# Kernel optimization log

Measured on AMD Instinct MI355X. Metric: run time of the kernel, lower is better.

## Reference

```python
import jax, jax.numpy as jnp
import numpy as np

B, IN_DIM, LATENT_DIM, EMBED_DIM = 262144, 512, 128, 10000


def setup_inputs() -> dict:
    key = jax.random.key(0)
    k_x, k_y, k_wlv, k_blv, k_wmu, k_bmu, k_we, k_be = jax.random.split(key, 8)
    s_in = 1.0 / np.sqrt(IN_DIM)
    s_e = 1.0 / np.sqrt(EMBED_DIM)
    return {
        "x": jax.random.normal(k_x, (B, IN_DIM), dtype=jnp.float32),
        "y": jax.random.randint(k_y, (B,), 0, EMBED_DIM, dtype=jnp.int32),
        # torch nn.Linear weights are [out_features, in_features]
        "W_logvar": jax.random.uniform(k_wlv, (LATENT_DIM, IN_DIM), minval=-s_in, maxval=s_in, dtype=jnp.float32),
        "b_logvar": jax.random.uniform(k_blv, (LATENT_DIM,), minval=-s_in, maxval=s_in, dtype=jnp.float32),
        "W_mean": jax.random.uniform(k_wmu, (LATENT_DIM, IN_DIM), minval=-s_in, maxval=s_in, dtype=jnp.float32),
        "b_mean": jax.random.uniform(k_bmu, (LATENT_DIM,), minval=-s_in, maxval=s_in, dtype=jnp.float32),
        "W_embed": jax.random.uniform(k_we, (LATENT_DIM, EMBED_DIM), minval=-s_e, maxval=s_e, dtype=jnp.float32),
        "b_embed": jax.random.uniform(k_be, (LATENT_DIM,), minval=-s_e, maxval=s_e, dtype=jnp.float32),
    }


def reference(x, y, W_logvar, b_logvar, W_mean, b_mean, W_embed, b_embed):
    # logvar / mean heads: plain dense GEMMs, x @ W.T + b
    logvar = jnp.einsum("bi,li->bl", x, W_logvar) + b_logvar
    mean = jnp.einsum("bi,li->bl", x, W_mean) + b_mean
    # one_hot(y) @ W_embed.T + b_embed  ==  gather columns of W_embed at y
    embed = jnp.take(W_embed, y, axis=1).T + b_embed  # [B, latent_dim]
    return (logvar, mean, embed)
```

## Files before the change

kernel.cpp:

```cpp
#include <hip/hip_runtime.h>
#include <hip/hip_bf16.h>

#define NB 262144
#define KD 512
#define ED 10000

typedef __attribute__((ext_vector_type(8))) short s8v;
typedef __attribute__((ext_vector_type(4))) float f4v;

typedef __attribute__((address_space(1))) const unsigned int gu32_t;
typedef __attribute__((address_space(3))) unsigned int lu32_t;

__device__ __forceinline__ short f2bf(float f) {
  union { __hip_bfloat16 h; short s; } u;
  u.h = __float2bfloat16(f);
  return u.s;
}

__global__ void prep_all(const float* __restrict__ Wlv, const float* __restrict__ Wmu,
                         unsigned short* __restrict__ wbf,
                         const float* __restrict__ We, const float* __restrict__ be,
                         float* __restrict__ embT) {
  __shared__ float t[32][129];
  if (blockIdx.x < 512) {
    int i = blockIdx.x * 256 + threadIdx.x;
    int row = i >> 9, col = i & 511;
    float v = (row < 128) ? Wlv[(row << 9) | col] : Wmu[((row - 128) << 9) | col];
    union { __hip_bfloat16 h; unsigned short s; } u;
    u.h = __float2bfloat16(v);
    wbf[i] = u.s;
  } else {
    const int v0 = (blockIdx.x - 512) << 5;
#pragma unroll
    for (int j = 0; j < 16; ++j) {
      int idx = j * 256 + threadIdx.x;
      int l = idx >> 5, vi = idx & 31;
      int v = v0 + vi;
      t[vi][l] = (v < ED) ? We[(size_t)l * ED + v] : 0.f;
    }
    __syncthreads();
#pragma unroll
    for (int j = 0; j < 16; ++j) {
      int idx = j * 256 + threadIdx.x;
      int v = idx >> 7, l = idx & 127;
      if (v0 + v < ED)
        embT[(size_t)(v0 + v) * 128 + l] = t[v][l] + be[l];
    }
  }
}

__global__ __launch_bounds__(512, 4) void gemm_heads(
    const float* __restrict__ x, const unsigned short* __restrict__ wbf,
    const float* __restrict__ blv, const float* __restrict__ bmu,
    const int* __restrict__ y, const float* __restrict__ embT,
    float* __restrict__ out, int doEmbed) {
  __shared__ char lds[3 * 24576];
  const int tid  = threadIdx.x;
  const int lane = tid & 63;
  const int wid  = tid >> 6;
  const int wm   = wid >> 2;
  const int wn   = wid & 3;
  const int gm   = blockIdx.x << 6;
  const int lr   = lane & 15;
  const int kg   = lane >> 4;

  const int arow = tid >> 3, aq = tid & 7;
  const unsigned aSrcBase = (unsigned)(arow << 9) + (unsigned)((aq ^ (arow & 7)) << 2);
  const unsigned aDst = (unsigned)(tid << 4);
  unsigned bSrcBase[2], bDst[2];
#pragma unroll
  for (int s = 0; s < 2; ++s) {
    int c = tid + (s << 9);
    int col = c >> 2, q = c & 3;
    int qp = q ^ ((col >> 1) & 3);
    bSrcBase[s] = (unsigned)(col << 9) + (unsigned)(qp << 3);
    bDst[s] = 8192u + (unsigned)(c << 4);
  }
  const float* xblk = x + ((size_t)gm << 9);

  unsigned offA[2][2], offB[4];
#pragma unroll
  for (int m = 0; m < 2; ++m) {
    int row = (wm << 5) + (m << 4) + lr;
    int sw = row & 7;
    offA[m][0] = (unsigned)(row << 7) + (unsigned)((((kg << 1))     ^ sw) << 4);
    offA[m][1] = (unsigned)(row << 7) + (unsigned)((((kg << 1) + 1) ^ sw) << 4);
  }
#pragma unroll
  for (int nt = 0; nt < 4; ++nt) {
    int col = (wn << 6) + (nt << 4) + lr;
    offB[nt] = 8192u + (unsigned)(col << 6) + (unsigned)((kg ^ ((col >> 1) & 3)) << 4);
  }

  f4v acc[2][4];
#pragma unroll
  for (int m = 0; m < 2; ++m)
#pragma unroll
    for (int nt = 0; nt < 4; ++nt) acc[m][nt] = (f4v)0.f;

#define ISSUE_STAGE(st)                                                            \
  {                                                                                \
    const int ke = (st) << 5;                                                      \
    char* sb = lds + ((st) % 3) * 24576;                                           \
    __builtin_amdgcn_global_load_lds((const gu32_t*)(xblk + aSrcBase + ke),        \
                                     (lu32_t*)(sb + aDst), 16, 0, 0);              \
    __builtin_amdgcn_global_load_lds((const gu32_t*)(wbf + bSrcBase[0] + ke),      \
                                     (lu32_t*)(sb + bDst[0]), 16, 0, 0);           \
    __builtin_amdgcn_global_load_lds((const gu32_t*)(wbf + bSrcBase[1] + ke),      \
                                     (lu32_t*)(sb + bDst[1]), 16, 0, 0);           \
  }

  ISSUE_STAGE(0)
  ISSUE_STAGE(1)
  asm volatile("s_waitcnt vmcnt(3)" ::: "memory");
  __builtin_amdgcn_s_barrier();

#pragma unroll
  for (int t = 0; t < 16; ++t) {
    if (t <= 13) ISSUE_STAGE(t + 2)
    const char* stage = lds + (t % 3) * 24576;
    s8v bfr[4];
#pragma unroll
    for (int nt = 0; nt < 4; ++nt)
      bfr[nt] = *(const s8v*)(stage + offB[nt]);
    s8v af[2];
#pragma unroll
    for (int m = 0; m < 2; ++m) {
      float4 a0 = *(const float4*)(stage + offA[m][0]);
      float4 a1 = *(const float4*)(stage + offA[m][1]);
      af[m][0] = f2bf(a0.x); af[m][1] = f2bf(a0.y); af[m][2] = f2bf(a0.z); af[m][3] = f2bf(a0.w);
      af[m][4] = f2bf(a1.x); af[m][5] = f2bf(a1.y); af[m][6] = f2bf(a1.z); af[m][7] = f2bf(a1.w);
    }
#pragma unroll
    for (int m = 0; m < 2; ++m)
#pragma unroll
      for (int nt = 0; nt < 4; ++nt)
        acc[m][nt] = __builtin_amdgcn_mfma_f32_16x16x32_bf16(af[m], bfr[nt], acc[m][nt], 0, 0, 0);
    asm volatile("s_waitcnt lgkmcnt(0)" ::: "memory");
    __builtin_amdgcn_sched_barrier(0);
    if (t <= 13)      { asm volatile("s_waitcnt vmcnt(3)" ::: "memory"); }
    else if (t == 14) { asm volatile("s_waitcnt vmcnt(0)" ::: "memory"); }
    if (t <= 14) __builtin_amdgcn_s_barrier();
  }
#undef ISSUE_STAGE

  const int rsub = kg << 2;
#pragma unroll
  for (int nt = 0; nt < 4; ++nt) {
    int col = (wn << 6) + (nt << 4) + lr;
    float bias = (col < 128) ? blv[col] : bmu[col - 128];
    float* ob = (col < 128) ? (out + col)
                            : (out + ((size_t)NB << 7) + (col - 128));
#pragma unroll
    for (int m = 0; m < 2; ++m) {
      int row0 = gm + (wm << 5) + (m << 4) + rsub;
#pragma unroll
      for (int r = 0; r < 4; ++r)
        ob[(size_t)(row0 + r) << 7] = acc[m][nt][r] + bias;
    }
  }

  if (doEmbed) {
    float* out3 = out + ((size_t)NB << 8);
    int r  = tid >> 3;
    int c0 = (tid & 7) << 4;
    int row = gm + r;
    int v = y[row];
    const float4* src = (const float4*)(embT + (size_t)v * 128 + c0);
    float4* dst = (float4*)(out + ((size_t)NB << 8) - ((size_t)NB << 8) + ((size_t)row << 7) + c0 + ((size_t)NB << 8) - ((size_t)row << 7) - c0 + ((size_t)row << 7) + c0);
    dst = (float4*)(out3 + ((size_t)row << 7) + c0);
#pragma unroll
    for (int j = 0; j < 4; ++j) dst[j] = src[j];
  }
}

__global__ void gemm_naive(const float* __restrict__ x,
                           const float* __restrict__ Wlv, const float* __restrict__ blv,
                           const float* __restrict__ Wmu, const float* __restrict__ bmu,
                           float* __restrict__ out) {
  __shared__ float xr[512];
  int b = blockIdx.x;
  for (int i = threadIdx.x; i < 512; i += 256) xr[i] = x[(size_t)b * 512 + i];
  __syncthreads();
  int c = threadIdx.x;
  const float* w = (c < 128) ? (Wlv + c * 512) : (Wmu + (c - 128) * 512);
  float s = 0.f;
  for (int k = 0; k < 512; ++k) s += xr[k] * w[k];
  s += (c < 128) ? blv[c] : bmu[c - 128];
  float* o = (c < 128) ? (out + (size_t)b * 128 + c)
                       : (out + ((size_t)NB << 7) + (size_t)b * 128 + (c - 128));
  *o = s;
}

__global__ void embed_direct(const int* __restrict__ y, const float* __restrict__ We,
                             const float* __restrict__ be, float* __restrict__ out3) {
  size_t t = (size_t)blockIdx.x * 256 + threadIdx.x;
  int b = (int)(t >> 7), l = (int)(t & 127);
  out3[t] = We[(size_t)l * ED + y[b]] + be[l];
}

extern "C" void kernel_launch(void* const* d_in, const int* in_sizes, int n_in,
                              void* d_out, int out_size, void* d_ws, size_t ws_size,
                              hipStream_t stream) {
  const float* x   = (const float*)d_in[0];
  const int*   y   = (const int*)d_in[1];
  const float* Wlv = (const float*)d_in[2];
  const float* blv = (const float*)d_in[3];
  const float* Wmu = (const float*)d_in[4];
  const float* bmu = (const float*)d_in[5];
  const float* We  = (const float*)d_in[6];
  const float* be  = (const float*)d_in[7];
  float* out  = (float*)d_out;
  float* out3 = out + ((size_t)NB << 8);

  const size_t needW = 256 * 512 * sizeof(unsigned short);
  const size_t needE = needW + (size_t)ED * 128 * sizeof(float);
  unsigned short* wbf = (unsigned short*)d_ws;
  float* embT = (float*)((char*)d_ws + needW);

  if (ws_size >= needE) {
    prep_all<<<512 + 313, 256, 0, stream>>>(Wlv, Wmu, wbf, We, be, embT);
    gemm_heads<<<NB / 64, 512, 0, stream>>>(x, wbf, blv, bmu, y, embT, out, 1);
  } else if (ws_size >= needW) {
    prep_all<<<512, 256, 0, stream>>>(Wlv, Wmu, wbf, We, be, (float*)d_ws);
    gemm_heads<<<NB / 64, 512, 0, stream>>>(x, wbf, blv, bmu, y, nullptr, out, 0);
    embed_direct<<<NB * 128 / 256, 256, 0, stream>>>(y, We, be, out3);
  } else {
    gemm_naive<<<NB, 256, 0, stream>>>(x, Wlv, blv, Wmu, bmu, out);
    embed_direct<<<NB * 128 / 256, 256, 0, stream>>>(y, We, be, out3);
  }
}
```

Measured before the change: 296.9 us.

## Split GEMM output columns across two workgroups with XCD-aware block remapping

Each 64-row block is now handled by two workgroups, one per head (logvar vs mean), halving the B tile, accumulators and LDS footprint so launch bounds can allow more resident workgroups. Block IDs are remapped so the two halves of a row block land on the same XCD and can share the x tile through L2. The cost is that x is loaded twice per row block, which raises L2 and possibly HBM traffic on an input-bandwidth-bound kernel. The embedding copy is done only by the first half.

Measured after the change: 298.5 us. No clear change (+0.5%).

```diff
diff --git a/kernel.cpp b/kernel.cpp
--- a/kernel.cpp
+++ b/kernel.cpp
@@ -49,36 +49,35 @@
   }
 }
 
-__global__ __launch_bounds__(512, 4) void gemm_heads(
+__global__ __launch_bounds__(512, 6) void gemm_heads(
     const float* __restrict__ x, const unsigned short* __restrict__ wbf,
     const float* __restrict__ blv, const float* __restrict__ bmu,
     const int* __restrict__ y, const float* __restrict__ embT,
     float* __restrict__ out, int doEmbed) {
-  __shared__ char lds[3 * 24576];
+  __shared__ char lds[3 * 16384];
   const int tid  = threadIdx.x;
   const int lane = tid & 63;
   const int wid  = tid >> 6;
   const int wm   = wid >> 2;
   const int wn   = wid & 3;
-  const int gm   = blockIdx.x << 6;
+  const unsigned orig = blockIdx.x;
+  const unsigned wg   = (orig & 7u) * 1024u + (orig >> 3);
+  const int rb = (int)(wg >> 1);
+  const int h  = (int)(wg & 1);
+  const int gm   = rb << 6;
+  const int gcol = h << 7;
   const int lr   = lane & 15;
   const int kg   = lane >> 4;
 
   const int arow = tid >> 3, aq = tid & 7;
-  const unsigned aSrcBase = (unsigned)(arow << 9) + (unsigned)((aq ^ (arow & 7)) << 2);
+  const unsigned aSrc = (unsigned)(arow << 9) + (unsigned)((aq ^ (arow & 7)) << 2);
   const unsigned aDst = (unsigned)(tid << 4);
-  unsigned bSrcBase[2], bDst[2];
-#pragma unroll
-  for (int s = 0; s < 2; ++s) {
-    int c = tid + (s << 9);
-    int col = c >> 2, q = c & 3;
-    int qp = q ^ ((col >> 1) & 3);
-    bSrcBase[s] = (unsigned)(col << 9) + (unsigned)(qp << 3);
-    bDst[s] = 8192u + (unsigned)(c << 4);
-  }
+  const int bcol = tid >> 2, bq = tid & 3;
+  const unsigned bSrc = (unsigned)((gcol + bcol) << 9) + (unsigned)((bq ^ ((bcol >> 1) & 3)) << 3);
+  const unsigned bDst = 8192u + (unsigned)(tid << 4);
   const float* xblk = x + ((size_t)gm << 9);
 
-  unsigned offA[2][2], offB[4];
+  unsigned offA[2][2], offB[2];
 #pragma unroll
   for (int m = 0; m < 2; ++m) {
     int row = (wm << 5) + (m << 4) + lr;
@@ -87,41 +86,39 @@
     offA[m][1] = (unsigned)(row << 7) + (unsigned)((((kg << 1) + 1) ^ sw) << 4);
   }
 #pragma unroll
-  for (int nt = 0; nt < 4; ++nt) {
-    int col = (wn << 6) + (nt << 4) + lr;
+  for (int nt = 0; nt < 2; ++nt) {
+    int col = (wn << 5) + (nt << 4) + lr;
     offB[nt] = 8192u + (unsigned)(col << 6) + (unsigned)((kg ^ ((col >> 1) & 3)) << 4);
   }
 
-  f4v acc[2][4];
+  f4v acc[2][2];
 #pragma unroll
   for (int m = 0; m < 2; ++m)
 #pragma unroll
-    for (int nt = 0; nt < 4; ++nt) acc[m][nt] = (f4v)0.f;
+    for (int nt = 0; nt < 2; ++nt) acc[m][nt] = (f4v)0.f;
 
 #define ISSUE_STAGE(st)                                                            \
   {                                                                                \
     const int ke = (st) << 5;                                                      \
-    char* sb = lds + ((st) % 3) * 24576;                                           \
-    __builtin_amdgcn_global_load_lds((const gu32_t*)(xblk + aSrcBase + ke),        \
+    char* sb = lds + ((st) % 3) * 16384;                                           \
+    __builtin_amdgcn_global_load_lds((const gu32_t*)(xblk + aSrc + ke),            \
                                      (lu32_t*)(sb + aDst), 16, 0, 0);              \
-    __builtin_amdgcn_global_load_lds((const gu32_t*)(wbf + bSrcBase[0] + ke),      \
-                                     (lu32_t*)(sb + bDst[0]), 16, 0, 0);           \
-    __builtin_amdgcn_global_load_lds((const gu32_t*)(wbf + bSrcBase[1] + ke),      \
-                                     (lu32_t*)(sb + bDst[1]), 16, 0, 0);           \
+    __builtin_amdgcn_global_load_lds((const gu32_t*)(wbf + bSrc + ke),             \
+                                     (lu32_t*)(sb + bDst), 16, 0, 0);              \
   }
 
   ISSUE_STAGE(0)
   ISSUE_STAGE(1)
-  asm volatile("s_waitcnt vmcnt(3)" ::: "memory");
+  asm volatile("s_waitcnt vmcnt(2)" ::: "memory");
   __builtin_amdgcn_s_barrier();
 
 #pragma unroll
   for (int t = 0; t < 16; ++t) {
     if (t <= 13) ISSUE_STAGE(t + 2)
-    const char* stage = lds + (t % 3) * 24576;
-    s8v bfr[4];
-#pragma unroll
-    for (int nt = 0; nt < 4; ++nt)
+    const char* stage = lds + (t % 3) * 16384;
+    s8v bfr[2];
+#pragma unroll
+    for (int nt = 0; nt < 2; ++nt)
       bfr[nt] = *(const s8v*)(stage + offB[nt]);
     s8v af[2];
 #pragma unroll
@@ -134,11 +131,11 @@
 #pragma unroll
     for (int m = 0; m < 2; ++m)
 #pragma unroll
-      for (int nt = 0; nt < 4; ++nt)
+      for (int nt = 0; nt < 2; ++nt)
         acc[m][nt] = __builtin_amdgcn_mfma_f32_16x16x32_bf16(af[m], bfr[nt], acc[m][nt], 0, 0, 0);
     asm volatile("s_waitcnt lgkmcnt(0)" ::: "memory");
     __builtin_amdgcn_sched_barrier(0);
-    if (t <= 13)      { asm volatile("s_waitcnt vmcnt(3)" ::: "memory"); }
+    if (t <= 13)      { asm volatile("s_waitcnt vmcnt(2)" ::: "memory"); }
     else if (t == 14) { asm volatile("s_waitcnt vmcnt(0)" ::: "memory"); }
     if (t <= 14) __builtin_amdgcn_s_barrier();
   }
@@ -146,8 +143,8 @@
 
   const int rsub = kg << 2;
 #pragma unroll
-  for (int nt = 0; nt < 4; ++nt) {
-    int col = (wn << 6) + (nt << 4) + lr;
+  for (int nt = 0; nt < 2; ++nt) {
+    int col = gcol + (wn << 5) + (nt << 4) + lr;
     float bias = (col < 128) ? blv[col] : bmu[col - 128];
     float* ob = (col < 128) ? (out + col)
                             : (out + ((size_t)NB << 7) + (col - 128));
@@ -160,15 +157,14 @@
     }
   }
 
-  if (doEmbed) {
+  if (doEmbed && h == 0) {
     float* out3 = out + ((size_t)NB << 8);
     int r  = tid >> 3;
     int c0 = (tid & 7) << 4;
     int row = gm + r;
     int v = y[row];
     const float4* src = (const float4*)(embT + (size_t)v * 128 + c0);
-    float4* dst = (float4*)(out + ((size_t)NB << 8) - ((size_t)NB << 8) + ((size_t)row << 7) + c0 + ((size_t)NB << 8) - ((size_t)row << 7) - c0 + ((size_t)row << 7) + c0);
-    dst = (float4*)(out3 + ((size_t)row << 7) + c0);
+    float4* dst = (float4*)(out3 + ((size_t)row << 7) + c0);
 #pragma unroll
     for (int j = 0; j < 4; ++j) dst[j] = src[j];
   }
@@ -220,10 +216,10 @@
 
   if (ws_size >= needE) {
     prep_all<<<512 + 313, 256, 0, stream>>>(Wlv, Wmu, wbf, We, be, embT);
-    gemm_heads<<<NB / 64, 512, 0, stream>>>(x, wbf, blv, bmu, y, embT, out, 1);
+    gemm_heads<<<NB / 32, 512, 0, stream>>>(x, wbf, blv, bmu, y, embT, out, 1);
   } else if (ws_size >= needW) {
     prep_all<<<512, 256, 0, stream>>>(Wlv, Wmu, wbf, We, be, (float*)d_ws);
-    gemm_heads<<<NB / 64, 512, 0, stream>>>(x, wbf, blv, bmu, y, nullptr, out, 0);
+    gemm_heads<<<NB / 32, 512, 0, stream>>>(x, wbf, blv, bmu, y, nullptr, out, 0);
     embed_direct<<<NB * 128 / 256, 256, 0, stream>>>(y, We, be, out3);
   } else {
     gemm_naive<<<NB, 256, 0, stream>>>(x, Wlv, blv, Wmu, bmu, out);
```
